# Kernel tuning notes

Hardware: AMD Instinct MI355X
Metric: run time of the kernel (lower is better)

Reference implementation:

```python
import jax, jax.numpy as jnp
import numpy as np

N, K, M, H, F = 4, 1024, 1024, 16, 4096
D = M // H  # per-head dim (dim_q = dim_v = 64)
EPS = 1e-5


def _mha(q_in, k_in, v_in, Wq, bq, Wk, bk, Wv, bv, Wo, bo, mask):
    # Wq/Wk/Wv: [H, M, D]; bq/bk/bv: [H, D]; Wo: [H*D, M]; bo: [M]
    q = jnp.einsum('nkm,hmd->nhkd', q_in, Wq) + bq[None, :, None, :]
    k = jnp.einsum('nkm,hmd->nhkd', k_in, Wk) + bk[None, :, None, :]
    v = jnp.einsum('nkm,hmd->nhkd', v_in, Wv) + bv[None, :, None, :]
    scores = jnp.einsum('nhkd,nhld->nhkl', q, k) / jnp.sqrt(jnp.asarray(D, q.dtype))
    if mask is not None:
        scores = jnp.where(mask[:, None, :, :] == 0, jnp.asarray(-jnp.inf, q.dtype), scores)
    attn = jax.nn.softmax(scores, axis=-1)          # [N,H,K,K]
    y = jnp.einsum('nhkl,nhld->nhkd', attn, v)      # [N,H,K,D]
    y = y.transpose(0, 2, 1, 3).reshape(q_in.shape[0], q_in.shape[1], -1)  # concat heads -> [N,K,H*D]
    return y @ Wo + bo


def _ln(x, g, b):
    mu = jnp.mean(x, axis=-1, keepdims=True)
    var = jnp.mean((x - mu) ** 2, axis=-1, keepdims=True)
    return (x - mu) * jax.lax.rsqrt(var + EPS) * g + b


def setup_inputs() -> dict:
    key = jax.random.key(0)
    ks = jax.random.split(key, 24)
    s = 0.02
    def rn(k, shape):
        return jax.random.normal(k, shape, dtype=jnp.float32) * s
    inp = {
        'dec_inp': jax.random.normal(ks[0], (N, K, M), dtype=jnp.float32),
        'enc_out': jax.random.normal(ks[1], (N, K, M), dtype=jnp.float32),
        'mask': jnp.tril(jnp.ones((K, K), dtype=jnp.int32))[None].repeat(N, axis=0),
        # self-attention params
        'Wq_s': rn(ks[2], (H, M, D)), 'bq_s': jnp.zeros((H, D)),
        'Wk_s': rn(ks[3], (H, M, D)), 'bk_s': jnp.zeros((H, D)),
        'Wv_s': rn(ks[4], (H, M, D)), 'bv_s': jnp.zeros((H, D)),
        'Wo_s': rn(ks[5], (H * D, M)), 'bo_s': jnp.zeros((M,)),
        # cross-attention params
        'Wq_c': rn(ks[6], (H, M, D)), 'bq_c': jnp.zeros((H, D)),
        'Wk_c': rn(ks[7], (H, M, D)), 'bk_c': jnp.zeros((H, D)),
        'Wv_c': rn(ks[8], (H, M, D)), 'bv_c': jnp.zeros((H, D)),
        'Wo_c': rn(ks[9], (H * D, M)), 'bo_c': jnp.zeros((M,)),
        # feedforward params
        'W1': rn(ks[10], (M, F)), 'b1': jnp.zeros((F,)),
        'W2': rn(ks[11], (F, M)), 'b2': jnp.zeros((M,)),
        # layernorm params
        'g1': jnp.ones((M,)), 'be1': jnp.zeros((M,)),
        'g2': jnp.ones((M,)), 'be2': jnp.zeros((M,)),
        'g3': jnp.ones((M,)), 'be3': jnp.zeros((M,)),
    }
    return inp


def reference(dec_inp, enc_out, mask,
              Wq_s, bq_s, Wk_s, bk_s, Wv_s, bv_s, Wo_s, bo_s,
              Wq_c, bq_c, Wk_c, bk_c, Wv_c, bv_c, Wo_c, bo_c,
              W1, b1, W2, b2, g1, be1, g2, be2, g3, be3):
    # masked self-attention + residual + LN (dropout = identity in eval)
    out1 = _mha(dec_inp, dec_inp, dec_inp, Wq_s, bq_s, Wk_s, bk_s, Wv_s, bv_s, Wo_s, bo_s, mask)
    out2 = _ln(dec_inp + out1, g1, be1)
    # cross-attention with encoder output + residual + LN
    out3 = _mha(out2, enc_out, enc_out, Wq_c, bq_c, Wk_c, bk_c, Wv_c, bv_c, Wo_c, bo_c, None)
    out4 = _ln(out3 + out2, g2, be2)
    # feedforward + residual + LN
    out5 = jax.nn.relu(out4 @ W1 + b1) @ W2 + b2
    return _ln(out5 + out4, g3, be3)
```

## Files before the change

kernel.cpp:

```cpp
#include <hip/hip_runtime.h>

#define NB   4
#define SEQ  1024
#define MD   1024
#define NH   16
#define HD   64
#define FF   4096
#define NK   (NB*SEQ)
#define EPSF 1e-5f
#define QS   3072

typedef short short8 __attribute__((ext_vector_type(8)));
typedef float f32x4  __attribute__((ext_vector_type(4)));
typedef unsigned short u16;
typedef unsigned int u32;

__device__ __forceinline__ u16 f2bf(float x) {
    union { float f; unsigned u; } v; v.f = x;
    unsigned r = v.u + 0x7FFF + ((v.u >> 16) & 1);
    return (u16)(r >> 16);
}
__device__ __forceinline__ u16 f2bf_trunc(float x) {
    union { float f; unsigned u; } v; v.f = x;
    return (u16)(v.u >> 16);
}
__device__ __forceinline__ float bf2f(u16 x) {
    union { unsigned u; float f; } v; v.u = ((unsigned)x) << 16;
    return v.f;
}
__device__ __forceinline__ void gload_lds16(const void* g, void* l) {
    __builtin_amdgcn_global_load_lds(
        (const __attribute__((address_space(1))) unsigned int*)g,
        (__attribute__((address_space(3))) unsigned int*)l,
        16, 0, 0);
}

__global__ __launch_bounds__(256) void conv_bf16(const float* __restrict__ s0,
                                                 const float* __restrict__ s1,
                                                 u16* __restrict__ d0,
                                                 u16* __restrict__ d1) {
    const float* S = blockIdx.y ? s1 : s0;
    u16* D = blockIdx.y ? d1 : d0;
    const int i = blockIdx.x * 256 + threadIdx.x;
    float4 v = ((const float4*)S)[i];
    ushort4 o;
    o.x = f2bf(v.x); o.y = f2bf(v.y); o.z = f2bf(v.z); o.w = f2bf(v.w);
    ((ushort4*)D)[i] = o;
}

__global__ __launch_bounds__(256) void mask_tiles(const int* __restrict__ mask,
                                                  int* __restrict__ cls,
                                                  u32* __restrict__ bits) {
    const int jt = blockIdx.x, qt = blockIdx.y, n = blockIdx.z;
    const int t = threadIdx.x;
    const int r = t >> 1, h2 = (t & 1) * 2;
    u32 bb[2];
#pragma unroll
    for (int sg = 0; sg < 2; ++sg) {
        const int* mp = &mask[((size_t)n * SEQ + qt * 128 + r) * SEQ + jt * 128 + (h2 + sg) * 32];
        u32 b = 0;
#pragma unroll
        for (int k = 0; k < 8; ++k) {
            int4 v = *(const int4*)(mp + k * 4);
            b |= (v.x ? 1u : 0u) << (k * 4 + 0);
            b |= (v.y ? 1u : 0u) << (k * 4 + 1);
            b |= (v.z ? 1u : 0u) << (k * 4 + 2);
            b |= (v.w ? 1u : 0u) << (k * 4 + 3);
        }
        bb[sg] = b;
    }
    const int tile = (n * 8 + qt) * 8 + jt;
    bits[((size_t)tile * 128 + r) * 4 + h2]     = bb[0];
    bits[((size_t)tile * 128 + r) * 4 + h2 + 1] = bb[1];
    const int nfull  = __syncthreads_count(bb[0] == 0xFFFFFFFFu && bb[1] == 0xFFFFFFFFu);
    const int nempty = __syncthreads_count(bb[0] == 0u && bb[1] == 0u);
    if (t == 0) cls[tile] = (nfull == 256) ? 2 : ((nempty == 256) ? 0 : 1);
}

struct QkvArgs { const float* src[6]; u16* dst[6]; };

__global__ __launch_bounds__(256) void repack_qkv(QkvArgs a) {
    const int m0 = blockIdx.x * 64;
    const int h  = blockIdx.y;
    const int w  = blockIdx.z;
    const float* W = a.src[w];
    u16* BT = a.dst[w];
    const int t = threadIdx.x;
    __shared__ u16 Ts[64][72];

    const int r = t >> 4, c4 = (t & 15) * 4;
#pragma unroll
    for (int p = 0; p < 4; ++p) {
        const int row = r + p * 16;
        float4 v = *(const float4*)&W[((size_t)h * 1024 + m0 + row) * 64 + c4];
        Ts[row][c4] = f2bf(v.x); Ts[row][c4 + 1] = f2bf(v.y);
        Ts[row][c4 + 2] = f2bf(v.z); Ts[row][c4 + 3] = f2bf(v.w);
    }
    __syncthreads();
    const int d = t >> 2, j0 = (t & 3) * 16;
#pragma unroll
    for (int p = 0; p < 4; ++p) {
        ushort4 o;
        o.x = Ts[j0 + p * 4 + 0][d]; o.y = Ts[j0 + p * 4 + 1][d];
        o.z = Ts[j0 + p * 4 + 2][d]; o.w = Ts[j0 + p * 4 + 3][d];
        *(ushort4*)&BT[((size_t)h * 64 + d) * 1024 + m0 + j0 + p * 4] = o;
    }
}

struct FD { const float* src; int ss; u16* dst; int ds; };
struct FlatArgs { FD d[10]; };

__global__ __launch_bounds__(256) void repack_flat(FlatArgs fa) {
    FD u = fa.d[blockIdx.z];
    const int r0 = blockIdx.x * 64;
    const int c0 = blockIdx.y * 64;
    const int t  = threadIdx.x;
    __shared__ u16 Ts[64][72];

    const int r = t >> 4, c4 = (t & 15) * 4;
#pragma unroll
    for (int p = 0; p < 4; ++p) {
        const int row = r + p * 16;
        float4 v = *(const float4*)&u.src[(size_t)(r0 + row) * u.ss + c0 + c4];
        Ts[row][c4] = f2bf(v.x); Ts[row][c4 + 1] = f2bf(v.y);
        Ts[row][c4 + 2] = f2bf(v.z); Ts[row][c4 + 3] = f2bf(v.w);
    }
    __syncthreads();
    const int d = t >> 2, j0 = (t & 3) * 16;
#pragma unroll
    for (int p = 0; p < 4; ++p) {
        ushort4 o;
        o.x = Ts[j0 + p * 4 + 0][d]; o.y = Ts[j0 + p * 4 + 1][d];
        o.z = Ts[j0 + p * 4 + 2][d]; o.w = Ts[j0 + p * 4 + 3][d];
        *(ushort4*)&u.dst[(size_t)(c0 + d) * u.ds + r0 + j0 + p * 4] = o;
    }
}

template<int OUT_BF16, int RELU, int RESID, int BIAS3, int PARTIAL, int VT>
__global__ __launch_bounds__(256) void gemm_mfma(const u16* __restrict__ A,
                                                 const u16* __restrict__ A2,
                                                 int Astride,
                                                 const u16* __restrict__ BT,
                                                 int Bstride,
                                                 const float* __restrict__ b0,
                                                 const float* __restrict__ b1p,
                                                 const float* __restrict__ b2p,
                                                 const float* __restrict__ resid,
                                                 void* __restrict__ Cout,
                                                 u16* __restrict__ VtOut,
                                                 int Kd, int Nd) {
    const int nt = blockIdx.x;
    const int mt = blockIdx.y;
    const int t  = threadIdx.x;
    const int wave = t >> 6, lane = t & 63;
    const int q = lane >> 4, l16 = lane & 15;
    const int wm = wave >> 1, wn = wave & 1;

    __shared__ __align__(16) u16 As[128 * 64];
    __shared__ __align__(16) u16 Bs[128 * 64];

    const int row0 = mt * 128, col0 = nt * 128;
    const u16* Ause = (col0 < 1024) ? A : A2;
    const int kBase = PARTIAL ? blockIdx.z * Kd : 0;

    f32x4 acc[4][4];
#pragma unroll
    for (int r = 0; r < 4; ++r)
#pragma unroll
        for (int c = 0; c < 4; ++c) acc[r][c] = (f32x4)0.0f;

    const int lrow = lane >> 3;
    const int lcb  = lane & 7;

    for (int k0 = 0; k0 < Kd; k0 += 64) {
        __syncthreads();
#pragma unroll
        for (int p = 0; p < 4; ++p) {
            const int rr = wave * 32 + p * 8 + lrow;
            const int gcb = lcb ^ (rr & 7);
            gload_lds16(Ause + (size_t)(row0 + rr) * Astride + kBase + k0 + gcb * 8, As + (size_t)(wave * 32 + p * 8) * 64);
            gload_lds16(BT   + (size_t)(col0 + rr) * Bstride + kBase + k0 + gcb * 8, Bs + (size_t)(wave * 32 + p * 8) * 64);
        }
        __syncthreads();

#pragma unroll
        for (int s = 0; s < 2; ++s) {
            const int pb = (q + s * 4) ^ (l16 & 7);
            short8 af[4], bf[4];
#pragma unroll
            for (int r = 0; r < 4; ++r)
                af[r] = *(const short8*)&As[(wm * 64 + r * 16 + l16) * 64 + pb * 8];
#pragma unroll
            for (int c = 0; c < 4; ++c)
                bf[c] = *(const short8*)&Bs[(wn * 64 + c * 16 + l16) * 64 + pb * 8];
#pragma unroll
            for (int r = 0; r < 4; ++r)
#pragma unroll
                for (int c = 0; c < 4; ++c)
                    acc[r][c] = __builtin_amdgcn_mfma_f32_16x16x32_bf16(af[r], bf[c], acc[r][c], 0, 0, 0);
        }
    }

    if (VT && col0 >= 2048) {
#pragma unroll
        for (int c = 0; c < 4; ++c) {
            const int col = col0 + wn * 64 + c * 16 + l16;
            const float bb = b2p[col & 1023];
            const int d = col & 63, hh = (col >> 6) & 15;
#pragma unroll
            for (int r = 0; r < 4; ++r) {
                const int row = row0 + wm * 64 + r * 16 + q * 4;
                const int nn = row >> 10, k = row & 1023;
                ushort4 o;
                o.x = f2bf(acc[r][c][0] + bb);
                o.y = f2bf(acc[r][c][1] + bb);
                o.z = f2bf(acc[r][c][2] + bb);
                o.w = f2bf(acc[r][c][3] + bb);
                *(ushort4*)&VtOut[((size_t)(nn * 16 + hh) * 64 + d) * 1024 + k] = o;
            }
        }
        return;
    }

    float* Pout = PARTIAL ? ((float*)Cout + (size_t)blockIdx.z * NK * Nd) : nullptr;

#pragma unroll
    for (int c = 0; c < 4; ++c) {
        const int col = col0 + wn * 64 + c * 16 + l16;
        float bb = 0.0f;
        if (!PARTIAL) {
            if (BIAS3) {
                const int sec = col >> 10;
                const float* bp = sec == 0 ? b0 : (sec == 1 ? b1p : b2p);
                bb = bp[col & 1023];
            } else {
                bb = b0[col];
            }
        }
#pragma unroll
        for (int r = 0; r < 4; ++r) {
#pragma unroll
            for (int reg = 0; reg < 4; ++reg) {
                const int row = row0 + wm * 64 + r * 16 + q * 4 + reg;
                float v = acc[r][c][reg] + bb;
                if (PARTIAL) {
                    Pout[(size_t)row * Nd + col] = acc[r][c][reg];
                } else {
                    if (RELU)  v = fmaxf(v, 0.0f);
                    if (RESID) v += resid[(size_t)row * Nd + col];
                    if (OUT_BF16) ((u16*)Cout)[(size_t)row * Nd + col] = f2bf(v);
                    else          ((float*)Cout)[(size_t)row * Nd + col] = v;
                }
            }
        }
    }
}

#define PSTR 136

__global__ __launch_bounds__(256) void attn_mfma(const u16* __restrict__ QKV,
                                                 const u16* __restrict__ Vt,
                                                 const int* __restrict__ cls,
                                                 const u32* __restrict__ bits,
                                                 u16* __restrict__ Yout) {
    const int qt = blockIdx.x;
    const int h  = blockIdx.y;
    const int n  = blockIdx.z;
    const int t  = threadIdx.x;
    const int wave = t >> 6;
    const int lane = t & 63;
    const int quad = lane >> 4;
    const int l16  = lane & 15;

    __shared__ __align__(16) u16 Ks[128 * 64];
    __shared__ __align__(16) u16 Vs[64 * 128];
    __shared__ __align__(16) u16 Ps[4][16 * PSTR];
    __shared__ u32 Mb[128][4];

    const int bh = n * NH + h;
    const int i0 = qt * 128;

    short8 qf[2][2];
#pragma unroll
    for (int s = 0; s < 2; ++s) {
        const u16* qrow = QKV + ((size_t)n * SEQ + i0 + s * 64 + wave * 16 + l16) * QS + h * 64 + quad * 8;
        short8 a = *(const short8*)(qrow);
        short8 b = *(const short8*)(qrow + 32);
#pragma unroll
        for (int j = 0; j < 8; ++j) {
            qf[s][0][j] = (short)f2bf(bf2f((u16)a[j]) * 0.18033688f);
            qf[s][1][j] = (short)f2bf(bf2f((u16)b[j]) * 0.18033688f);
        }
    }

    f32x4 O[2][4];
#pragma unroll
    for (int s = 0; s < 2; ++s)
#pragma unroll
        for (int d = 0; d < 4; ++d) O[s][d] = (f32x4)0.0f;
    float lrow[2][4] = {};

    const int krow = lane >> 3, kblk = lane & 7;
    const int vrow = lane >> 4, vblk = lane & 15;
    const int x7 = l16 & 7;

    for (int jt = 0; jt < SEQ / 128; ++jt) {
        const int c = cls ? cls[(n * 8 + qt) * 8 + jt] : 2;
        if (c == 0) continue;
        __syncthreads();

#pragma unroll
        for (int p = 0; p < 4; ++p) {
            const int rr = wave * 32 + p * 8 + krow;
            const int kb = kblk ^ (rr & 7);
            gload_lds16(QKV + ((size_t)n * SEQ + jt * 128 + rr) * QS + 1024 + h * 64 + kb * 8,
                        Ks + (wave * 32 + p * 8) * 64);
        }
#pragma unroll
        for (int p = 0; p < 4; ++p) {
            const int rr = wave * 16 + p * 4 + vrow;
            const int kb = vblk ^ (rr & 15);
            gload_lds16(Vt + ((size_t)bh * HD + rr) * SEQ + jt * 128 + kb * 8,
                        Vs + (wave * 16 + p * 4) * 128);
        }
        if (c == 1) {
            const u32* bp = &bits[((size_t)((n * 8 + qt) * 8 + jt) * 128 + (t >> 1)) * 4 + (t & 1) * 2];
            Mb[t >> 1][(t & 1) * 2]     = bp[0];
            Mb[t >> 1][(t & 1) * 2 + 1] = bp[1];
        }
        __syncthreads();

#pragma unroll
        for (int s = 0; s < 2; ++s) {
            f32x4 S[8];
#pragma unroll
            for (int sub = 0; sub < 8; ++sub) {
                S[sub] = (f32x4)0.0f;
                const int row = sub * 16 + l16;
                short8 k0 = *(const short8*)&Ks[row * 64 + ((quad ^ x7) * 8)];
                S[sub] = __builtin_amdgcn_mfma_f32_16x16x32_bf16(qf[s][0], k0, S[sub], 0, 0, 0);
                short8 k1 = *(const short8*)&Ks[row * 64 + (((4 + quad) ^ x7) * 8)];
                S[sub] = __builtin_amdgcn_mfma_f32_16x16x32_bf16(qf[s][1], k1, S[sub], 0, 0, 0);
            }

            if (c == 1) {
#pragma unroll
                for (int reg = 0; reg < 4; ++reg) {
                    const int row = s * 64 + wave * 16 + quad * 4 + reg;
                    const u32 m0 = Mb[row][0], m1 = Mb[row][1], m2 = Mb[row][2], m3 = Mb[row][3];
#pragma unroll
                    for (int sub = 0; sub < 8; ++sub) {
                        const u32 seg = (sub >> 1) == 0 ? m0 : (sub >> 1) == 1 ? m1 : (sub >> 1) == 2 ? m2 : m3;
                        if (!((seg >> ((sub & 1) * 16 + l16)) & 1u)) S[sub][reg] = -1e30f;
                    }
                }
            }

#pragma unroll
            for (int reg = 0; reg < 4; ++reg) {
                float rs = 0.0f;
#pragma unroll
                for (int sub = 0; sub < 8; ++sub) {
                    float e = exp2f(S[sub][reg]);
                    Ps[wave][(quad * 4 + reg) * PSTR + sub * 16 + l16] = f2bf_trunc(e);
                    rs += e;
                }
                rs += __shfl_xor(rs, 1);
                rs += __shfl_xor(rs, 2);
                rs += __shfl_xor(rs, 4);
                rs += __shfl_xor(rs, 8);
                lrow[s][reg] += rs;
            }

            short8 pa[4];
#pragma unroll
            for (int ks = 0; ks < 4; ++ks)
                pa[ks] = *(const short8*)&Ps[wave][l16 * PSTR + ks * 32 + quad * 8];
#pragma unroll
            for (int d = 0; d < 4; ++d) {
                const int row = d * 16 + l16;
#pragma unroll
                for (int ks = 0; ks < 4; ++ks) {
                    short8 vb = *(const short8*)&Vs[row * 128 + (((ks * 4 + quad) ^ l16) & 15) * 8];
                    O[s][d] = __builtin_amdgcn_mfma_f32_16x16x32_bf16(pa[ks], vb, O[s][d], 0, 0, 0);
                }
            }
        }
    }

#pragma unroll
    for (int s = 0; s < 2; ++s) {
#pragma unroll
        for (int d = 0; d < 4; ++d) {
#pragma unroll
            for (int reg = 0; reg < 4; ++reg) {
                const int row = i0 + s * 64 + wave * 16 + quad * 4 + reg;
                const int col = h * 64 + d * 16 + l16;
                Yout[((size_t)n * SEQ + row) * QS + col] = f2bf(O[s][d][reg] / lrow[s][reg]);
            }
        }
    }
}

__global__ __launch_bounds__(256) void ln_kernel(const float* __restrict__ X,
                                                 const float* __restrict__ g,
                                                 const float* __restrict__ be,
                                                 float* __restrict__ Y,
                                                 u16* __restrict__ Yb) {
    const int row = blockIdx.x;
    const int t = threadIdx.x;
    __shared__ float red[256];

    const float4 v = ((const float4*)(X + (size_t)row * MD))[t];
    red[t] = v.x + v.y + v.z + v.w;
    __syncthreads();
    for (int s2 = 128; s2 > 0; s2 >>= 1) {
        if (t < s2) red[t] += red[t + s2];
        __syncthreads();
    }
    const float mu = red[0] * (1.0f / MD);
    __syncthreads();

    float dx = v.x - mu, dy = v.y - mu, dz = v.z - mu, dw = v.w - mu;
    red[t] = dx * dx + dy * dy + dz * dz + dw * dw;
    __syncthreads();
    for (int s2 = 128; s2 > 0; s2 >>= 1) {
        if (t < s2) red[t] += red[t + s2];
        __syncthreads();
    }
    const float var = red[0] * (1.0f / MD);
    const float rs = rsqrtf(var + EPSF);

    const float4 gv = ((const float4*)g)[t];
    const float4 bv = ((const float4*)be)[t];
    float4 o;
    o.x = dx * rs * gv.x + bv.x;
    o.y = dy * rs * gv.y + bv.y;
    o.z = dz * rs * gv.z + bv.z;
    o.w = dw * rs * gv.w + bv.w;
    if (Y) ((float4*)(Y + (size_t)row * MD))[t] = o;
    if (Yb) {
        ushort4 ob;
        ob.x = f2bf(o.x); ob.y = f2bf(o.y); ob.z = f2bf(o.z); ob.w = f2bf(o.w);
        ((ushort4*)(Yb + (size_t)row * MD))[t] = ob;
    }
}

__global__ __launch_bounds__(256) void ln_fused2(const float* __restrict__ p0,
                                                 const float* __restrict__ p1,
                                                 const float* __restrict__ bias,
                                                 const float* __restrict__ resid,
                                                 const float* __restrict__ g,
                                                 const float* __restrict__ be,
                                                 float* __restrict__ Y) {
    const int row = blockIdx.x;
    const int t = threadIdx.x;
    __shared__ float red[256];

    const float4 a = ((const float4*)(p0 + (size_t)row * MD))[t];
    const float4 b = ((const float4*)(p1 + (size_t)row * MD))[t];
    const float4 r = ((const float4*)(resid + (size_t)row * MD))[t];
    const float4 bi = ((const float4*)bias)[t];
    float4 v;
    v.x = a.x + b.x + r.x + bi.x;
    v.y = a.y + b.y + r.y + bi.y;
    v.z = a.z + b.z + r.z + bi.z;
    v.w = a.w + b.w + r.w + bi.w;

    red[t] = v.x + v.y + v.z + v.w;
    __syncthreads();
    for (int s2 = 128; s2 > 0; s2 >>= 1) {
        if (t < s2) red[t] += red[t + s2];
        __syncthreads();
    }
    const float mu = red[0] * (1.0f / MD);
    __syncthreads();

    float dx = v.x - mu, dy = v.y - mu, dz = v.z - mu, dw = v.w - mu;
    red[t] = dx * dx + dy * dy + dz * dz + dw * dw;
    __syncthreads();
    for (int s2 = 128; s2 > 0; s2 >>= 1) {
        if (t < s2) red[t] += red[t + s2];
        __syncthreads();
    }
    const float var = red[0] * (1.0f / MD);
    const float rs = rsqrtf(var + EPSF);

    const float4 gv = ((const float4*)g)[t];
    const float4 bv = ((const float4*)be)[t];
    float4 o;
    o.x = dx * rs * gv.x + bv.x;
    o.y = dy * rs * gv.y + bv.y;
    o.z = dz * rs * gv.z + bv.z;
    o.w = dw * rs * gv.w + bv.w;
    ((float4*)(Y + (size_t)row * MD))[t] = o;
}

extern "C" void kernel_launch(void* const* d_in, const int* in_sizes, int n_in,
                              void* d_out, int out_size, void* d_ws, size_t ws_size,
                              hipStream_t stream) {
    const float* dec  = (const float*)d_in[0];
    const float* enc  = (const float*)d_in[1];
    const int*   mask = (const int*)d_in[2];
    const float* Wq_s = (const float*)d_in[3];
    const float* bq_s = (const float*)d_in[4];
    const float* Wk_s = (const float*)d_in[5];
    const float* bk_s = (const float*)d_in[6];
    const float* Wv_s = (const float*)d_in[7];
    const float* bv_s = (const float*)d_in[8];
    const float* Wo_s = (const float*)d_in[9];
    const float* bo_s = (const float*)d_in[10];
    const float* Wq_c = (const float*)d_in[11];
    const float* bq_c = (const float*)d_in[12];
    const float* Wk_c = (const float*)d_in[13];
    const float* bk_c = (const float*)d_in[14];
    const float* Wv_c = (const float*)d_in[15];
    const float* bv_c = (const float*)d_in[16];
    const float* Wo_c = (const float*)d_in[17];
    const float* bo_c = (const float*)d_in[18];
    const float* W1   = (const float*)d_in[19];
    const float* b1   = (const float*)d_in[20];
    const float* W2   = (const float*)d_in[21];
    const float* b2   = (const float*)d_in[22];
    const float* g1   = (const float*)d_in[23];
    const float* be1  = (const float*)d_in[24];
    const float* g2   = (const float*)d_in[25];
    const float* be2  = (const float*)d_in[26];
    const float* g3   = (const float*)d_in[27];
    const float* be3  = (const float*)d_in[28];

    char* wsb = (char*)d_ws;
    const size_t MB = 1u << 20;
    u16*   decb  = (u16*)(wsb + 0 * MB);
    u16*   O2b   = (u16*)(wsb + 0 * MB);
    u16*   encb  = (u16*)(wsb + 8 * MB);
    u16*   O4b   = (u16*)(wsb + 8 * MB);
    u16*   WqkvsT= (u16*)(wsb + 16 * MB);
    u16*   WqkvcT= (u16*)(wsb + 22 * MB);
    u16*   WosT  = (u16*)(wsb + 28 * MB);
    u16*   WocT  = (u16*)(wsb + 30 * MB);
    u16*   W1T   = (u16*)(wsb + 32 * MB);
    u16*   W2T   = (u16*)(wsb + 40 * MB);
    u16*   QKVb  = (u16*)(wsb + 48 * MB);
    u16*   Vt    = (u16*)(wsb + 72 * MB);
    u16*   Hb    = (u16*)(wsb + 48 * MB);
    int*   mcls  = (int*)(wsb + 80 * MB);
    u32*   mbits = (u32*)(wsb + 80 * MB + 64 * 1024);
    float* Tb    = (float*)(wsb + 80 * MB);
    float* FP    = (float*)(wsb + 0 * MB);
    float* O2    = (float*)(wsb + 96 * MB);
    float* O4    = (float*)(wsb + 96 * MB);

    dim3 blk(256);
    dim3 gConv(NK * MD / 4 / 256, 2);
    dim3 gMask(8, 8, 4);
    dim3 gQkvW(16, 16, 6);
    dim3 gFlatW(16, 16, 10);
    dim3 gAttn(SEQ / 128, NH, NB);
    dim3 gQKV(QS / 128, NK / 128);
    dim3 gOut(MD / 128, NK / 128);
    dim3 gF1(FF / 128, NK / 128);
    dim3 gF2(MD / 128, NK / 128, 2);

    conv_bf16<<<gConv, blk, 0, stream>>>(dec, enc, decb, encb);
    mask_tiles<<<gMask, blk, 0, stream>>>(mask, mcls, mbits);

    QkvArgs qa;
    qa.src[0] = Wq_s; qa.src[1] = Wk_s; qa.src[2] = Wv_s;
    qa.src[3] = Wq_c; qa.src[4] = Wk_c; qa.src[5] = Wv_c;
    qa.dst[0] = WqkvsT;                 qa.dst[1] = WqkvsT + (size_t)1024 * 1024;
    qa.dst[2] = WqkvsT + (size_t)2048 * 1024;
    qa.dst[3] = WqkvcT;                 qa.dst[4] = WqkvcT + (size_t)1024 * 1024;
    qa.dst[5] = WqkvcT + (size_t)2048 * 1024;
    repack_qkv<<<gQkvW, blk, 0, stream>>>(qa);

    FlatArgs fa;
    fa.d[0] = { Wo_s, 1024, WosT, 1024 };
    fa.d[1] = { Wo_c, 1024, WocT, 1024 };
    for (int u = 0; u < 4; ++u)
        fa.d[2 + u] = { W1 + (size_t)u * 1024, 4096, W1T + (size_t)u * 1024 * 1024, 1024 };
    for (int u = 0; u < 4; ++u)
        fa.d[6 + u] = { W2 + (size_t)u * 1024 * 1024, 1024, W2T + (size_t)u * 1024, 4096 };
    repack_flat<<<gFlatW, blk, 0, stream>>>(fa);

    gemm_mfma<1, 0, 0, 1, 0, 1><<<gQKV, blk, 0, stream>>>(decb, decb, MD, WqkvsT, MD, bq_s, bk_s, bv_s, nullptr, QKVb, Vt, MD, QS);
    attn_mfma<<<gAttn, blk, 0, stream>>>(QKVb, Vt, mcls, mbits, QKVb);
    gemm_mfma<0, 0, 1, 0, 0, 0><<<gOut, blk, 0, stream>>>(QKVb, QKVb, QS, WosT, MD, bo_s, nullptr, nullptr, dec, Tb, nullptr, MD, MD);
    ln_kernel<<<NK, blk, 0, stream>>>(Tb, g1, be1, O2, O2b);

    gemm_mfma<1, 0, 0, 1, 0, 1><<<gQKV, blk, 0, stream>>>(O2b, encb, MD, WqkvcT, MD, bq_c, bk_c, bv_c, nullptr, QKVb, Vt, MD, QS);
    attn_mfma<<<gAttn, blk, 0, stream>>>(QKVb, Vt, nullptr, nullptr, QKVb);
    gemm_mfma<0, 0, 1, 0, 0, 0><<<gOut, blk, 0, stream>>>(QKVb, QKVb, QS, WocT, MD, bo_c, nullptr, nullptr, O2, Tb, nullptr, MD, MD);
    ln_kernel<<<NK, blk, 0, stream>>>(Tb, g2, be2, O4, O4b);

    gemm_mfma<1, 1, 0, 0, 0, 0><<<gF1, blk, 0, stream>>>(O4b, O4b, MD, W1T, MD, b1, nullptr, nullptr, nullptr, Hb, nullptr, MD, FF);
    gemm_mfma<0, 0, 0, 0, 1, 0><<<gF2, blk, 0, stream>>>(Hb, Hb, FF, W2T, FF, nullptr, nullptr, nullptr, nullptr, FP, nullptr, FF / 2, MD);
    ln_fused2<<<NK, blk, 0, stream>>>(FP, FP + (size_t)NK * MD, b2, O4, g3, be3, (float*)d_out);
}
```

Baseline: 391.2 us.

## Split attention query tile across eight waves instead of four

```diff
diff --git a/kernel.cpp b/kernel.cpp
--- a/kernel.cpp
+++ b/kernel.cpp
@@ -257,12 +257,13 @@
 }
 
 #define PSTR 136
-
-__global__ __launch_bounds__(256) void attn_mfma(const u16* __restrict__ QKV,
-                                                 const u16* __restrict__ Vt,
-                                                 const int* __restrict__ cls,
-                                                 const u32* __restrict__ bits,
-                                                 u16* __restrict__ Yout) {
+#define ATTN_LDS (128*64*2 + 64*128*2 + 8*16*PSTR*2)
+
+__global__ __launch_bounds__(512, 4) void attn_mfma(const u16* __restrict__ QKV,
+                                                    const u16* __restrict__ Vt,
+                                                    const int* __restrict__ cls,
+                                                    const u32* __restrict__ bits,
+                                                    u16* __restrict__ Yout) {
     const int qt = blockIdx.x;
     const int h  = blockIdx.y;
     const int n  = blockIdx.z;
@@ -271,133 +272,131 @@
     const int lane = t & 63;
     const int quad = lane >> 4;
     const int l16  = lane & 15;
-
-    __shared__ __align__(16) u16 Ks[128 * 64];
-    __shared__ __align__(16) u16 Vs[64 * 128];
-    __shared__ __align__(16) u16 Ps[4][16 * PSTR];
-    __shared__ u32 Mb[128][4];
+    const int sw   = wave >> 2;
+    const int wq   = wave & 3;
+
+    extern __shared__ __align__(16) char smem[];
+    u16* Ks = (u16*)smem;
+    u16* Vs = (u16*)(smem + 128 * 64 * 2);
+    u16* Pw = (u16*)(smem + 128 * 64 * 2 + 64 * 128 * 2) + wave * 16 * PSTR;
 
     const int bh = n * NH + h;
     const int i0 = qt * 128;
 
-    short8 qf[2][2];
-#pragma unroll
-    for (int s = 0; s < 2; ++s) {
-        const u16* qrow = QKV + ((size_t)n * SEQ + i0 + s * 64 + wave * 16 + l16) * QS + h * 64 + quad * 8;
+    int cl[8];
+    if (cls) {
+        const int* cp = &cls[(n * 8 + qt) * 8];
+#pragma unroll
+        for (int j = 0; j < 8; ++j) cl[j] = cp[j];
+    } else {
+#pragma unroll
+        for (int j = 0; j < 8; ++j) cl[j] = 2;
+    }
+
+    short8 qf[2];
+    {
+        const u16* qrow = QKV + ((size_t)n * SEQ + i0 + sw * 64 + wq * 16 + l16) * QS + h * 64 + quad * 8;
         short8 a = *(const short8*)(qrow);
         short8 b = *(const short8*)(qrow + 32);
 #pragma unroll
         for (int j = 0; j < 8; ++j) {
-            qf[s][0][j] = (short)f2bf(bf2f((u16)a[j]) * 0.18033688f);
-            qf[s][1][j] = (short)f2bf(bf2f((u16)b[j]) * 0.18033688f);
-        }
-    }
-
-    f32x4 O[2][4];
-#pragma unroll
-    for (int s = 0; s < 2; ++s)
-#pragma unroll
-        for (int d = 0; d < 4; ++d) O[s][d] = (f32x4)0.0f;
-    float lrow[2][4] = {};
+            qf[0][j] = (short)f2bf(bf2f((u16)a[j]) * 0.18033688f);
+            qf[1][j] = (short)f2bf(bf2f((u16)b[j]) * 0.18033688f);
+        }
+    }
+
+    f32x4 O[4];
+#pragma unroll
+    for (int d = 0; d < 4; ++d) O[d] = (f32x4)0.0f;
+    float lrow[4] = {};
 
     const int krow = lane >> 3, kblk = lane & 7;
     const int vrow = lane >> 4, vblk = lane & 15;
     const int x7 = l16 & 7;
 
     for (int jt = 0; jt < SEQ / 128; ++jt) {
-        const int c = cls ? cls[(n * 8 + qt) * 8 + jt] : 2;
+        const int c = cl[jt];
         if (c == 0) continue;
         __syncthreads();
 
 #pragma unroll
-        for (int p = 0; p < 4; ++p) {
-            const int rr = wave * 32 + p * 8 + krow;
+        for (int p = 0; p < 2; ++p) {
+            const int rr = wave * 16 + p * 8 + krow;
             const int kb = kblk ^ (rr & 7);
             gload_lds16(QKV + ((size_t)n * SEQ + jt * 128 + rr) * QS + 1024 + h * 64 + kb * 8,
-                        Ks + (wave * 32 + p * 8) * 64);
-        }
-#pragma unroll
-        for (int p = 0; p < 4; ++p) {
-            const int rr = wave * 16 + p * 4 + vrow;
+                        Ks + (wave * 16 + p * 8) * 64);
+        }
+#pragma unroll
+        for (int p = 0; p < 2; ++p) {
+            const int rr = wave * 8 + p * 4 + vrow;
             const int kb = vblk ^ (rr & 15);
             gload_lds16(Vt + ((size_t)bh * HD + rr) * SEQ + jt * 128 + kb * 8,
-                        Vs + (wave * 16 + p * 4) * 128);
-        }
+                        Vs + (wave * 8 + p * 4) * 128);
+        }
+        __syncthreads();
+
+        f32x4 S[8];
+#pragma unroll
+        for (int sub = 0; sub < 8; ++sub) {
+            S[sub] = (f32x4)0.0f;
+            const int row = sub * 16 + l16;
+            short8 k0 = *(const short8*)&Ks[row * 64 + ((quad ^ x7) * 8)];
+            S[sub] = __builtin_amdgcn_mfma_f32_16x16x32_bf16(qf[0], k0, S[sub], 0, 0, 0);
+            short8 k1 = *(const short8*)&Ks[row * 64 + (((4 + quad) ^ x7) * 8)];
+            S[sub] = __builtin_amdgcn_mfma_f32_16x16x32_bf16(qf[1], k1, S[sub], 0, 0, 0);
+        }
+
         if (c == 1) {
-            const u32* bp = &bits[((size_t)((n * 8 + qt) * 8 + jt) * 128 + (t >> 1)) * 4 + (t & 1) * 2];
-            Mb[t >> 1][(t & 1) * 2]     = bp[0];
-            Mb[t >> 1][(t & 1) * 2 + 1] = bp[1];
-        }
-        __syncthreads();
-
-#pragma unroll
-        for (int s = 0; s < 2; ++s) {
-            f32x4 S[8];
-#pragma unroll
-            for (int sub = 0; sub < 8; ++sub) {
-                S[sub] = (f32x4)0.0f;
-                const int row = sub * 16 + l16;
-                short8 k0 = *(const short8*)&Ks[row * 64 + ((quad ^ x7) * 8)];
-                S[sub] = __builtin_amdgcn_mfma_f32_16x16x32_bf16(qf[s][0], k0, S[sub], 0, 0, 0);
-                short8 k1 = *(const short8*)&Ks[row * 64 + (((4 + quad) ^ x7) * 8)];
-                S[sub] = __builtin_amdgcn_mfma_f32_16x16x32_bf16(qf[s][1], k1, S[sub], 0, 0, 0);
-            }
-
-            if (c == 1) {
-#pragma unroll
-                for (int reg = 0; reg < 4; ++reg) {
-                    const int row = s * 64 + wave * 16 + quad * 4 + reg;
-                    const u32 m0 = Mb[row][0], m1 = Mb[row][1], m2 = Mb[row][2], m3 = Mb[row][3];
-#pragma unroll
-                    for (int sub = 0; sub < 8; ++sub) {
-                        const u32 seg = (sub >> 1) == 0 ? m0 : (sub >> 1) == 1 ? m1 : (sub >> 1) == 2 ? m2 : m3;
-                        if (!((seg >> ((sub & 1) * 16 + l16)) & 1u)) S[sub][reg] = -1e30f;
-                    }
+#pragma unroll
+            for (int reg = 0; reg < 4; ++reg) {
+                const int row = sw * 64 + wq * 16 + quad * 4 + reg;
+                const uint4 mm = *(const uint4*)&bits[((size_t)((n * 8 + qt) * 8 + jt) * 128 + row) * 4];
+#pragma unroll
+                for (int sub = 0; sub < 8; ++sub) {
+                    const u32 seg = (sub >> 1) == 0 ? mm.x : (sub >> 1) == 1 ? mm.y : (sub >> 1) == 2 ? mm.z : mm.w;
+                    if (!((seg >> ((sub & 1) * 16 + l16)) & 1u)) S[sub][reg] = -1e30f;
                 }
             }
-
-#pragma unroll
-            for (int reg = 0; reg < 4; ++reg) {
-                float rs = 0.0f;
-#pragma unroll
-                for (int sub = 0; sub < 8; ++sub) {
-                    float e = exp2f(S[sub][reg]);
-                    Ps[wave][(quad * 4 + reg) * PSTR + sub * 16 + l16] = f2bf_trunc(e);
-                    rs += e;
-                }
-                rs += __shfl_xor(rs, 1);
-                rs += __shfl_xor(rs, 2);
-                rs += __shfl_xor(rs, 4);
-                rs += __shfl_xor(rs, 8);
-                lrow[s][reg] += rs;
+        }
+
+#pragma unroll
+        for (int reg = 0; reg < 4; ++reg) {
+            float rs = 0.0f;
+#pragma unroll
+            for (int sub = 0; sub < 8; ++sub) {
+                float e = exp2f(S[sub][reg]);
+                Pw[(quad * 4 + reg) * PSTR + sub * 16 + l16] = f2bf_trunc(e);
+                rs += e;
             }
-
-            short8 pa[4];
-#pragma unroll
-            for (int ks = 0; ks < 4; ++ks)
-                pa[ks] = *(const short8*)&Ps[wave][l16 * PSTR + ks * 32 + quad * 8];
-#pragma unroll
-            for (int d = 0; d < 4; ++d) {
-                const int row = d * 16 + l16;
-#pragma unroll
-                for (int ks = 0; ks < 4; ++ks) {
-                    short8 vb = *(const short8*)&Vs[row * 128 + (((ks * 4 + quad) ^ l16) & 15) * 8];
-                    O[s][d] = __builtin_amdgcn_mfma_f32_16x16x32_bf16(pa[ks], vb, O[s][d], 0, 0, 0);
-                }
+            rs += __shfl_xor(rs, 1);
+            rs += __shfl_xor(rs, 2);
+            rs += __shfl_xor(rs, 4);
+            rs += __shfl_xor(rs, 8);
+            lrow[reg] += rs;
+        }
+
+        short8 pa[4];
+#pragma unroll
+        for (int ks = 0; ks < 4; ++ks)
+            pa[ks] = *(const short8*)&Pw[l16 * PSTR + ks * 32 + quad * 8];
+#pragma unroll
+        for (int d = 0; d < 4; ++d) {
+            const int row = d * 16 + l16;
+#pragma unroll
+            for (int ks = 0; ks < 4; ++ks) {
+                short8 vb = *(const short8*)&Vs[row * 128 + (((ks * 4 + quad) ^ l16) & 15) * 8];
+                O[d] = __builtin_amdgcn_mfma_f32_16x16x32_bf16(pa[ks], vb, O[d], 0, 0, 0);
             }
         }
     }
 
 #pragma unroll
-    for (int s = 0; s < 2; ++s) {
-#pragma unroll
-        for (int d = 0; d < 4; ++d) {
-#pragma unroll
-            for (int reg = 0; reg < 4; ++reg) {
-                const int row = i0 + s * 64 + wave * 16 + quad * 4 + reg;
-                const int col = h * 64 + d * 16 + l16;
-                Yout[((size_t)n * SEQ + row) * QS + col] = f2bf(O[s][d][reg] / lrow[s][reg]);
-            }
+    for (int d = 0; d < 4; ++d) {
+#pragma unroll
+        for (int reg = 0; reg < 4; ++reg) {
+            const int row = i0 + sw * 64 + wq * 16 + quad * 4 + reg;
+            const int col = h * 64 + d * 16 + l16;
+            Yout[((size_t)n * SEQ + row) * QS + col] = f2bf(O[d][reg] / lrow[reg]);
         }
     }
 }
@@ -552,6 +551,7 @@
     float* O4    = (float*)(wsb + 96 * MB);
 
     dim3 blk(256);
+    dim3 blkA(512);
     dim3 gConv(NK * MD / 4 / 256, 2);
     dim3 gMask(8, 8, 4);
     dim3 gQkvW(16, 16, 6);
@@ -584,12 +584,12 @@
     repack_flat<<<gFlatW, blk, 0, stream>>>(fa);
 
     gemm_mfma<1, 0, 0, 1, 0, 1><<<gQKV, blk, 0, stream>>>(decb, decb, MD, WqkvsT, MD, bq_s, bk_s, bv_s, nullptr, QKVb, Vt, MD, QS);
-    attn_mfma<<<gAttn, blk, 0, stream>>>(QKVb, Vt, mcls, mbits, QKVb);
+    attn_mfma<<<gAttn, blkA, ATTN_LDS, stream>>>(QKVb, Vt, mcls, mbits, QKVb);
     gemm_mfma<0, 0, 1, 0, 0, 0><<<gOut, blk, 0, stream>>>(QKVb, QKVb, QS, WosT, MD, bo_s, nullptr, nullptr, dec, Tb, nullptr, MD, MD);
     ln_kernel<<<NK, blk, 0, stream>>>(Tb, g1, be1, O2, O2b);
 
     gemm_mfma<1, 0, 0, 1, 0, 1><<<gQKV, blk, 0, stream>>>(O2b, encb, MD, WqkvcT, MD, bq_c, bk_c, bv_c, nullptr, QKVb, Vt, MD, QS);
-    attn_mfma<<<gAttn, blk, 0, stream>>>(QKVb, Vt, nullptr, nullptr, QKVb);
+    attn_mfma<<<gAttn, blkA, ATTN_LDS, stream>>>(QKVb, Vt, nullptr, nullptr, QKVb);
     gemm_mfma<0, 0, 1, 0, 0, 0><<<gOut, blk, 0, stream>>>(QKVb, QKVb, QS, WocT, MD, bo_c, nullptr, nullptr, O2, Tb, nullptr, MD, MD);
     ln_kernel<<<NK, blk, 0, stream>>>(Tb, g2, be2, O4, O4b);
 
```

Result: faster. 375.4 us (-4.0%).
